# Optimization experiments

Hardware: AMD Instinct MI355X
Metric: run time of the kernel (lower is better)

## Reference

```python
import jax, jax.numpy as jnp
import numpy as np

B, C, H, W = 2, 256, 64, 64
HEADS, SR = 8, 4
D = C // HEADS          # head dim = 32
N = H * W               # query length = 4096
EPS = 1e-5


def _conv(x, w, stride=1, pad=0, groups=1, b=None):
    out = jax.lax.conv_general_dilated(
        x, w, (stride, stride), [(pad, pad), (pad, pad)],
        dimension_numbers=('NCHW', 'OIHW', 'NCHW'),
        feature_group_count=groups)
    if b is not None:
        out = out + b[None, :, None, None]
    return out


def _bn(x, p):
    # p: [4, C] = (gamma, beta, running_mean, running_var), eval-mode BN
    g, b, m, v = p[0], p[1], p[2], p[3]
    s = g / jnp.sqrt(v + EPS)
    return (x - m[None, :, None, None]) * s[None, :, None, None] + b[None, :, None, None]


def setup_inputs() -> dict:
    key = jax.random.key(0)
    ks = iter(jax.random.split(key, 32))
    nrm = lambda shape, s=0.05: jax.random.normal(next(ks), shape, jnp.float32) * s
    def bnp():
        return jnp.stack([jnp.ones((C,), jnp.float32), jnp.zeros((C,), jnp.float32),
                          jax.random.normal(next(ks), (C,), jnp.float32) * 0.1,
                          jax.random.uniform(next(ks), (C,), jnp.float32) + 0.5])
    return dict(
        x=jax.random.normal(next(ks), (B, C, H, W), jnp.float32),
        relative_pos_enc=jax.random.normal(next(ks), (B, 2, 64, 64), jnp.float32),
        q_w=nrm((C, C, 1, 1)), q_b=jnp.zeros((C,), jnp.float32),
        kv_w=nrm((2 * C, C, 1, 1)), kv_b=jnp.zeros((2 * C,), jnp.float32),
        sr1_dw_w=nrm((C, 1, SR + 3, SR + 3)), sr1_bn1=bnp(),
        sr1_pw_w=nrm((C, 1, 1, 1), 0.5), sr1_bn2=bnp(),
        sr2_dw_w=nrm((C, 1, SR // 2 + 3, SR // 2 + 3)), sr2_bn1=bnp(),
        sr2_pw_w=nrm((C, 1, 1, 1), 0.5), sr2_bn2=bnp(),
        local_w=nrm((C, 1, 3, 3)), local_b=jnp.zeros((C,), jnp.float32),
    )


def reference(x, relative_pos_enc, q_w, q_b, kv_w, kv_b,
              sr1_dw_w, sr1_bn1, sr1_pw_w, sr1_bn2,
              sr2_dw_w, sr2_bn1, sr2_pw_w, sr2_bn2,
              local_w, local_b):
    scale = D ** -0.5
    # q: 1x1 conv -> [B, heads, N, D]; both branches use the FIRST half of heads
    q = _conv(x, q_w, b=q_b).reshape(B, HEADS, D, N).transpose(0, 1, 3, 2)
    qh = q[:, :HEADS // 2]

    def branch(dw_w, bn1, pw_w, bn2, stride, pad, rpe_slice):
        # SR path: depthwise conv + BN + ReLU, depthwise 1x1 + BN
        y = jax.nn.relu(_bn(_conv(x, dw_w, stride, pad, groups=C), bn1))
        y = _bn(_conv(y, pw_w, groups=C), bn2)
        # local 3x3 depthwise mixing with residual
        y = _conv(y, local_w, pad=1, groups=C, b=local_b) + y
        kv = _conv(y, kv_w, b=kv_b)                # [B, 2C, h', w']
        k, v = jnp.split(kv, 2, axis=1)
        L = 2 * y.shape[2] * y.shape[3]            # channel-fold doubles kv length
        k = k.reshape(B, HEADS // 2, D, L)
        v = v.reshape(B, HEADS // 2, D, L).transpose(0, 1, 3, 2)
        attn = jnp.einsum('bhnd,bhdl->bhnl', qh, k) * scale
        rpe = jax.image.resize(rpe_slice, (B, 1, N, L), method='bicubic')
        attn = jax.nn.softmax(attn + rpe, axis=-1)
        return jnp.einsum('bhnl,bhld->bhnd', attn, v)

    x1 = branch(sr1_dw_w, sr1_bn1, sr1_pw_w, sr1_bn2,
                SR, (SR + 3) // 2, relative_pos_enc[:, 0:1])
    x2 = branch(sr2_dw_w, sr2_bn1, sr2_pw_w, sr2_bn2,
                SR // 2, (SR // 2 + 3) // 2, relative_pos_enc[:, 1:2])
    out = jnp.concatenate([x1, x2], axis=-1)       # [B, heads//2, N, 2D]
    return out.reshape(B, C, H, W)
```

## Files before the change

### kernel.cpp

```cpp
#include <hip/hip_runtime.h>
#include <hip/hip_bf16.h>
#include <math.h>

#define NB 2
#define NC 256
#define HWIN 4096
#define NN 4096
#define ND 32
#define NHH 4
#define EPSV 1e-5f

typedef short short8 __attribute__((ext_vector_type(8)));
typedef float f32x4 __attribute__((ext_vector_type(4)));
typedef unsigned short u16;
typedef unsigned int u32;

#define OFF_T1   0
#define OFF_T2   262144
#define OFF_Q    1310720
#define OFF_KT1  1835008
#define OFF_VT1  1900544
#define OFF_KT2  1966080
#define OFF_VT2  2228224
#define OFF_RCT1 2490368
#define OFF_RCT2 2531328
#define OFF_WT   2695168
#define OFF_QWT  5054464
#define OFF_LWP  5087232

#define QSCALE 0.2550437314857726f
#define LOG2E  1.4426950408889634f

__device__ __forceinline__ u16 f2bf(float x) {
  unsigned u = __float_as_uint(x);
  u += 0x7fffu + ((u >> 16) & 1u);
  return (u16)(u >> 16);
}

__device__ __forceinline__ u32 pk_bf16(float a, float b) {
  __hip_bfloat162 h = __float22bfloat162_rn(make_float2(a, b));
  u32 r; __builtin_memcpy(&r, &h, 4);
  return r;
}

__device__ __forceinline__ float keysw(float t) {
  t = fabsf(t);
  float w;
  if (t < 1.f)       w = ((1.5f*t - 2.5f)*t)*t + 1.f;
  else if (t < 2.f)  w = ((-0.5f*t + 2.5f)*t - 4.f)*t + 2.f;
  else               w = 0.f;
  return w;
}

template<int KS, int STR, int PAD, int OH>
__device__ __forceinline__ void dwconv_body(int idx, const float* __restrict__ x,
    const float* __restrict__ dww, const float* __restrict__ bn1,
    const float* __restrict__ pww, const float* __restrict__ bn2,
    float* __restrict__ tout) {
  const int hw = OH*OH;
  int s = idx % hw; int c = (idx/hw) % NC; int b = idx/(hw*NC);
  int oy = s / OH, ox = s % OH;
  const float* xp = x + (b*NC + c)*HWIN;
  const float* wp = dww + c*KS*KS;
  float acc = 0.f;
  #pragma unroll
  for (int ky = 0; ky < KS; ++ky) {
    int iy = oy*STR - PAD + ky;
    if (iy < 0 || iy >= 64) continue;
    #pragma unroll
    for (int kx = 0; kx < KS; ++kx) {
      int ix = ox*STR - PAD + kx;
      if (ix < 0 || ix >= 64) continue;
      acc += xp[iy*64 + ix] * wp[ky*KS + kx];
    }
  }
  float s1 = bn1[c] * rsqrtf(bn1[3*NC + c] + EPSV);
  float z = (acc - bn1[2*NC + c])*s1 + bn1[NC + c];
  z = fmaxf(z, 0.f);
  float s2 = bn2[c] * rsqrtf(bn2[3*NC + c] + EPSV);
  z = z * (pww[c]*s2) + (bn2[NC + c] - bn2[2*NC + c]*s2);
  tout[((size_t)(b*hw + s))*NC + c] = z;
}

__device__ __forceinline__ void rpe_body(int idx, const float* __restrict__ rpe,
                                         u16* __restrict__ rcT, int L, int ch) {
  int r = idx & 63; int l = (idx >> 6) % L; int b = idx / (64*L);
  float f = ((float)l + 0.5f)*(64.f/(float)L) - 0.5f;
  int i0 = (int)floorf(f) - 1;
  const float* rp = rpe + ((b*2 + ch)*64 + r)*64;
  float v = 0.f, wsum = 0.f;
  #pragma unroll
  for (int j = 0; j < 4; ++j) {
    int i = i0 + j;
    if (i >= 0 && i < 64) {
      float w = keysw(f - (float)i);
      v += w * rp[i]; wsum += w;
    }
  }
  rcT[((size_t)(b*L + l))*80 + 4 + r] = f2bf(v / wsum);
}

__global__ void __launch_bounds__(256) prep_kernel(
    const float* __restrict__ x,
    const float* __restrict__ dw1, const float* __restrict__ bn11,
    const float* __restrict__ pw1, const float* __restrict__ bn12, float* __restrict__ t1,
    const float* __restrict__ dw2, const float* __restrict__ bn21,
    const float* __restrict__ pw2, const float* __restrict__ bn22, float* __restrict__ t2,
    const float* __restrict__ kvw, float* __restrict__ wtp,
    const float* __restrict__ qw, float* __restrict__ qwp2,
    const float* __restrict__ lw, float* __restrict__ lwp) {
  int blk = blockIdx.x;
  int t = threadIdx.x;
  if (blk < 512) {
    dwconv_body<7,4,3,16>(blk*256 + t, x, dw1, bn11, pw1, bn12, t1);
  } else if (blk < 2560) {
    dwconv_body<5,2,2,32>((blk-512)*256 + t, x, dw2, bn21, pw2, bn22, t2);
  } else if (blk < 2688) {
    int idx = (blk-2560)*256 + t;
    float4 vv = *(const float4*)(kvw + (size_t)idx*4);
    int o = idx >> 6, c4 = idx & 63;
    *(float4*)(wtp + ((size_t)(c4*512 + o))*4) = vv;
  } else if (blk < 2720) {
    int idx = (blk-2688)*256 + t;
    float4 vv = *(const float4*)(qw + (size_t)idx*4);
    int oc = idx >> 6, c0 = (idx & 63)*4;
    int ocq = oc >> 2, r = oc & 3;
    qwp2[((size_t)((c0+0)*32 + ocq))*4 + r] = vv.x;
    qwp2[((size_t)((c0+1)*32 + ocq))*4 + r] = vv.y;
    qwp2[((size_t)((c0+2)*32 + ocq))*4 + r] = vv.z;
    qwp2[((size_t)((c0+3)*32 + ocq))*4 + r] = vv.w;
  } else {
    int c = t;
    #pragma unroll
    for (int tp = 0; tp < 9; ++tp) lwp[tp*256 + c] = lw[c*9 + tp];
  }
}

__global__ void __launch_bounds__(256) localkv_kernel(
    const float* __restrict__ t1T, const float* __restrict__ t2T,
    const float* __restrict__ lwp, const float* __restrict__ lb,
    const float* __restrict__ wtp, const float* __restrict__ kvb,
    u16* __restrict__ kt1, u16* __restrict__ vt1,
    u16* __restrict__ kt2, u16* __restrict__ vt2,
    const float* __restrict__ x, const float* __restrict__ qwp2,
    const float* __restrict__ qb, u16* __restrict__ q,
    const float* __restrict__ rpe, u16* __restrict__ rct1, u16* __restrict__ rct2) {
  __shared__ float sbuf[128*32];
  int blk = blockIdx.x, tid = threadIdx.x;
  if (blk < 640) {
    int kv = blk & 1, ti = blk >> 1;
    const float* tT; u16 *kT, *vT; int OH, hw, b, s0;
    if (ti < 64) { tT = t1T; kT = kt1; vT = vt1; OH = 16; hw = 256;  b = ti >> 5; s0 = (ti & 31)*8; }
    else { int v2 = ti-64; tT = t2T; kT = kt2; vT = vt2; OH = 32; hw = 1024; b = v2 >> 7; s0 = (v2 & 127)*8; }
    int oy = s0 / OH, ox0 = s0 % OH;
    const float* tb = tT + (size_t)b*hw*NC;
    int cl = tid & 63, spg = tid >> 6;
    int c0 = cl*4;
    f32x4 wt9[9];
    #pragma unroll
    for (int tp = 0; tp < 9; ++tp) wt9[tp] = *(const f32x4*)(lwp + tp*256 + c0);
    f32x4 lb4 = *(const f32x4*)(lb + c0);
    #pragma unroll
    for (int i = 0; i < 2; ++i) {
      int sp = spg*2 + i;
      int ox = ox0 + sp;
      f32x4 a = lb4;
      #pragma unroll
      for (int dy = 0; dy < 3; ++dy) {
        int iy = oy + dy - 1;
        if (iy < 0 || iy >= OH) continue;
        #pragma unroll
        for (int dx = 0; dx < 3; ++dx) {
          int ix = ox + dx - 1;
          if (ix < 0 || ix >= OH) continue;
          f32x4 tv = *(const f32x4*)(tb + (size_t)(iy*OH + ix)*NC + c0);
          a += tv * wt9[dy*3 + dx];
        }
      }
      a += *(const f32x4*)(tb + (size_t)(oy*OH + ox)*NC + c0);
      *(f32x4*)(sbuf + sp*NC + c0) = a;
    }
    __syncthreads();
    int ol = tid & 127, sph = tid >> 7;
    int o0i = kv*256 + ol, o1i = o0i + 128;
    float acc0[4], acc1[4];
    float b0 = kvb[o0i], b1 = kvb[o1i];
    #pragma unroll
    for (int i = 0; i < 4; ++i) { acc0[i] = b0; acc1[i] = b1; }
    #pragma unroll 2
    for (int c4 = 0; c4 < 64; ++c4) {
      f32x4 w0 = *(const f32x4*)(wtp + ((size_t)(c4*512 + o0i))*4);
      f32x4 w1 = *(const f32x4*)(wtp + ((size_t)(c4*512 + o1i))*4);
      #pragma unroll
      for (int i = 0; i < 4; ++i) {
        f32x4 y4 = *(const f32x4*)(sbuf + (sph*4 + i)*NC + c4*4);
        #pragma unroll
        for (int j = 0; j < 4; ++j) { acc0[i] += w0[j]*y4[j]; acc1[i] += w1[j]*y4[j]; }
      }
    }
    int L2 = 2*hw;
    #pragma unroll
    for (int k = 0; k < 2; ++k) {
      const float* ap = k ? acc1 : acc0;
      int oo = ol + k*128;
      int hh = oo >> 6, r = oo & 63, d = r >> 1, e = r & 1;
      if (kv == 0) {
        u16* kp = kT + ((size_t)((b*NHH + hh)*L2 + e*hw + s0 + sph*4))*ND + d;
        #pragma unroll
        for (int j = 0; j < 4; ++j) kp[j*ND] = f2bf(ap[j]);
      } else {
        int l0v = e*hw + s0 + sph*4;
        u16* vp = vT + ((size_t)((b*NHH + hh)*(L2/64) + (l0v >> 6))*ND + d)*64 + (l0v & 63);
        #pragma unroll
        for (int j = 0; j < 4; ++j) vp[j] = f2bf(ap[j]);
      }
    }
  } else if (blk < 896) {
    int qblk = blk - 640;
    int b = qblk >> 7;
    int n0 = (qblk & 127) * 32;
    const float* xb = x + (size_t)b*NC*HWIN + n0;
    int ocq = tid & 31, spg = tid >> 5;
    float acc[4][4];
    #pragma unroll
    for (int k = 0; k < 4; ++k) {
      float bias = qb[ocq*4 + k];
      #pragma unroll
      for (int i = 0; i < 4; ++i) acc[k][i] = bias;
    }
    #pragma unroll
    for (int half = 0; half < 2; ++half) {
      #pragma unroll
      for (int j = 0; j < 4; ++j) {
        int u = tid + 256*j;
        int c = u >> 3, spq = u & 7;
        *(f32x4*)(sbuf + c*32 + spq*4) =
            *(const f32x4*)(xb + (size_t)(half*128 + c)*HWIN + spq*4);
      }
      __syncthreads();
      #pragma unroll 4
      for (int c = 0; c < 128; ++c) {
        int cg = half*128 + c;
        f32x4 w4 = *(const f32x4*)(qwp2 + ((size_t)(cg*32 + ocq))*4);
        f32x4 y4 = *(const f32x4*)(sbuf + c*32 + spg*4);
        #pragma unroll
        for (int k = 0; k < 4; ++k)
          #pragma unroll
          for (int i = 0; i < 4; ++i) acc[k][i] += w4[k]*y4[i];
      }
      __syncthreads();
    }
    #pragma unroll
    for (int k = 0; k < 4; ++k) {
      int oc = ocq*4 + k;
      int h = oc >> 5, d = oc & 31;
      u16* qp = q + (((size_t)(b*NHH + h))*NN + n0 + spg*4)*ND + d;
      #pragma unroll
      for (int i = 0; i < 4; ++i) qp[i*ND] = f2bf(acc[k][i]*QSCALE);
    }
  } else if (blk < 1152) {
    rpe_body((blk-896)*256 + tid, rpe, rct1, 512, 0);
  } else {
    rpe_body((blk-1152)*256 + tid, rpe, rct2, 2048, 1);
  }
}

__global__ void __launch_bounds__(256) attn_kernel(
    const u16* __restrict__ qbf,
    const u16* __restrict__ kt1, const u16* __restrict__ vt1, const u16* __restrict__ rct1,
    const u16* __restrict__ kt2, const u16* __restrict__ vt2, const u16* __restrict__ rct2,
    float* __restrict__ out) {
  __shared__ u16 kbuf[64*32];
  __shared__ u16 vbuf[32*64];
  __shared__ u32 pbuf_all[4][16*32];
  int u = blockIdx.x;
  int b = u >> 8, hh = (u >> 6) & 3, rb = u & 63;
  int tid = threadIdx.x;
  int w = tid >> 6, lane = tid & 63;
  int g = lane >> 4, lo = lane & 15;
  u32* pbuf = pbuf_all[w];
  u16* pbuf16 = (u16*)pbuf;
  int n = rb*64 + w*16 + lo;

  short8 qf = *(const short8*)(qbf + (((size_t)(b*NHH + hh))*NN + n)*ND + 8*g);

  float fr = ((float)n + 0.5f)*(1.f/64.f) - 0.5f;
  int ri0 = (int)floorf(fr) - 1;
  int a = (w < 2) ? rb - 2 : rb - 1;
  int rmin = a & ~3;
  float wr4[4]; float wsum = 0.f;
  #pragma unroll
  for (int j = 0; j < 4; ++j) {
    int i = ri0 + j;
    float wv = (i >= 0 && i < 64) ? keysw(fr - (float)i) : 0.f;
    wr4[j] = wv; wsum += wv;
  }
  float invw = LOG2E / wsum;
  float wt8[8];
  #pragma unroll
  for (int s = 0; s < 8; ++s) {
    float acc = 0.f;
    #pragma unroll
    for (int j = 0; j < 4; ++j)
      acc += (ri0 + j - rmin == s) ? wr4[j]*invw : 0.f;
    wt8[s] = acc;
  }
  short8 wtf;
  {
    u32 p0 = pk_bf16(wt8[0], wt8[1]), p1 = pk_bf16(wt8[2], wt8[3]);
    u32 p2 = pk_bf16(wt8[4], wt8[5]), p3 = pk_bf16(wt8[6], wt8[7]);
    uint4 uu = make_uint4(p0, p1, p2, p3);
    wtf = __builtin_bit_cast(short8, uu);
    if (g != 0) wtf = (short8)0;
  }

  const f32x4 zero = {0.f, 0.f, 0.f, 0.f};

  int kr_row = tid >> 2, kr_col = (tid & 3)*8;
  int kr_sw  = ((kr_row >> 1) & 3)*8;
  int vr_row = tid >> 3, vr_col = (tid & 7)*8;
  int vr_sw  = (vr_row & 7)*8;
  int ksw = ((lo >> 1) & 3)*8;
  int vsw = (lo & 7)*8;
  int psw4 = (lo & 7)*4;
  int psw8 = (lo & 7)*8;

  for (int pass = 0; pass < 2; ++pass) {
    const int L  = pass ? 2048 : 512;
    const int nt = pass ? 32 : 8;
    const u16* kbase  = (pass ? kt2 : kt1) + (size_t)(b*NHH + hh)*L*ND;
    const u16* vbase  = (pass ? vt2 : vt1) + (size_t)(b*NHH + hh)*ND*L;
    const u16* rcrow0 = (pass ? rct2 : rct1) + (size_t)b*L*80 + (rmin + 4);

    auto stageLoad = [&](short8& kr, short8& vr, int l0) {
      kr = *(const short8*)(kbase + (size_t)(l0 + kr_row)*ND + kr_col);
      vr = *(const short8*)(vbase + (size_t)(l0 >> 6)*(ND*64) + vr_row*64 + vr_col);
    };
    auto stageStore = [&](short8 kr, short8 vr) {
      *(short8*)(kbuf + kr_row*32 + (kr_col ^ kr_sw)) = kr;
      *(short8*)(vbuf + vr_row*64 + (vr_col ^ vr_sw)) = vr;
    };
    auto loadRC = [&](uint4 (&rc)[4], int l0) {
      #pragma unroll
      for (int c = 0; c < 4; ++c) {
        const u16* arow = rcrow0 + (size_t)(l0 + 16*c + lo)*80;
        uint2 ra = *(const uint2*)arow;
        uint2 rb2 = *(const uint2*)(arow + 4);
        rc[c] = make_uint4(ra.x, ra.y, rb2.x, rb2.y);
      }
    };

    float ssum = 0.f;
    f32x4 o0 = zero, o1 = zero;
    short8 kr, vr;
    uint4 rcA[4], rcB[4];
    stageLoad(kr, vr, 0);
    loadRC(rcA, 0);

    for (int t = 0; t < nt; ++t) {
      stageStore(kr, vr);
      __syncthreads();
      if (t < nt-1) { stageLoad(kr, vr, (t+1)*64); loadRC(rcB, (t+1)*64); }
      f32x4 s4[4];
      #pragma unroll
      for (int c = 0; c < 4; ++c) {
        short8 rcf = __builtin_bit_cast(short8, rcA[c]);
        f32x4 accr = __builtin_amdgcn_mfma_f32_16x16x32_bf16(rcf, wtf, zero, 0, 0, 0);
        short8 kf = *(const short8*)(kbuf + (16*c + lo)*32 + ((8*g) ^ ksw));
        s4[c] = __builtin_amdgcn_mfma_f32_16x16x32_bf16(kf, qf, accr, 0, 0, 0);
      }
      float psum = 0.f;
      u32 pk[8];
      #pragma unroll
      for (int c = 0; c < 4; ++c) {
        float p0 = __builtin_amdgcn_exp2f(s4[c][0]);
        float p1 = __builtin_amdgcn_exp2f(s4[c][1]);
        float p2 = __builtin_amdgcn_exp2f(s4[c][2]);
        float p3 = __builtin_amdgcn_exp2f(s4[c][3]);
        psum += (p0 + p1) + (p2 + p3);
        pk[2*c]   = pk_bf16(p0, p1);
        pk[2*c+1] = pk_bf16(p2, p3);
      }
      ssum += psum;
      #pragma unroll
      for (int c = 0; c < 4; ++c)
        *(uint2*)(pbuf + lo*32 + ((8*c + 2*g) ^ psw4)) = make_uint2(pk[2*c], pk[2*c+1]);
      short8 pf0 = *(const short8*)(pbuf16 + lo*64 + ((8*g) ^ psw8));
      short8 pf1 = *(const short8*)(pbuf16 + lo*64 + ((32 + 8*g) ^ psw8));
      short8 v00 = *(const short8*)(vbuf + lo*64 + ((8*g) ^ vsw));
      short8 v01 = *(const short8*)(vbuf + lo*64 + ((32 + 8*g) ^ vsw));
      short8 v10 = *(const short8*)(vbuf + (16 + lo)*64 + ((8*g) ^ vsw));
      short8 v11 = *(const short8*)(vbuf + (16 + lo)*64 + ((32 + 8*g) ^ vsw));
      o0 = __builtin_amdgcn_mfma_f32_16x16x32_bf16(v00, pf0, o0, 0, 0, 0);
      o1 = __builtin_amdgcn_mfma_f32_16x16x32_bf16(v10, pf0, o1, 0, 0, 0);
      o0 = __builtin_amdgcn_mfma_f32_16x16x32_bf16(v01, pf1, o0, 0, 0, 0);
      o1 = __builtin_amdgcn_mfma_f32_16x16x32_bf16(v11, pf1, o1, 0, 0, 0);
      if (t < nt-1) {
        #pragma unroll
        for (int j = 0; j < 4; ++j) rcA[j] = rcB[j];
      }
      __syncthreads();
    }

    ssum += __shfl_xor(ssum, 16, 64);
    ssum += __shfl_xor(ssum, 32, 64);
    float inv = 1.f/ssum;
    f32x4 w0 = o0*inv, w1 = o1*inv;
    float* op = out + ((size_t)((b*NC + hh*64 + rb)*64 + (w*16 + lo)))*64 + pass*32;
    *(f32x4*)(op + 4*g)      = w0;
    *(f32x4*)(op + 16 + 4*g) = w1;
  }
}

extern "C" void kernel_launch(void* const* d_in, const int* in_sizes, int n_in,
                              void* d_out, int out_size, void* d_ws, size_t ws_size,
                              hipStream_t stream) {
  const float* x    = (const float*)d_in[0];
  const float* rpe  = (const float*)d_in[1];
  const float* qw   = (const float*)d_in[2];
  const float* qb   = (const float*)d_in[3];
  const float* kvw  = (const float*)d_in[4];
  const float* kvb  = (const float*)d_in[5];
  const float* dw1  = (const float*)d_in[6];
  const float* bn11 = (const float*)d_in[7];
  const float* pw1  = (const float*)d_in[8];
  const float* bn12 = (const float*)d_in[9];
  const float* dw2  = (const float*)d_in[10];
  const float* bn21 = (const float*)d_in[11];
  const float* pw2  = (const float*)d_in[12];
  const float* bn22 = (const float*)d_in[13];
  const float* lw   = (const float*)d_in[14];
  const float* lb   = (const float*)d_in[15];
  float* out = (float*)d_out;
  float* ws  = (float*)d_ws;

  float* t1   = ws + OFF_T1;
  float* t2   = ws + OFF_T2;
  u16*   q    = (u16*)(ws + OFF_Q);
  u16*   kt1  = (u16*)(ws + OFF_KT1);
  u16*   vt1  = (u16*)(ws + OFF_VT1);
  u16*   kt2  = (u16*)(ws + OFF_KT2);
  u16*   vt2  = (u16*)(ws + OFF_VT2);
  u16*   rct1 = (u16*)(ws + OFF_RCT1);
  u16*   rct2 = (u16*)(ws + OFF_RCT2);
  float* wtp  = ws + OFF_WT;
  float* qwp2 = ws + OFF_QWT;
  float* lwp  = ws + OFF_LWP;

  hipLaunchKernelGGL(prep_kernel, dim3(2721), dim3(256), 0, stream,
                     x, dw1, bn11, pw1, bn12, t1, dw2, bn21, pw2, bn22, t2,
                     kvw, wtp, qw, qwp2, lw, lwp);
  hipLaunchKernelGGL(localkv_kernel, dim3(2176), dim3(256), 0, stream,
                     t1, t2, lwp, lb, wtp, kvb, kt1, vt1, kt2, vt2, x, qwp2, qb, q,
                     rpe, rct1, rct2);
  hipLaunchKernelGGL(attn_kernel, dim3(512), dim3(256), 0, stream,
                     q, kt1, vt1, rct1, kt2, vt2, rct2, out);
}
```

Baseline: 180.5 us.

## Split attention kernel into per-branch 2-wave blocks for more parallelism

Each attention block used to process 64 queries with 4 waves and loop over both branches in sequence. Now each block handles 32 queries and a single branch with 2 waves, and the long branch's blocks are scheduled first. The grid grows from 512 to 2048 blocks, which should fill the GPU better and balance the uneven branch lengths. In exchange, each K/V tile is staged into shared memory by fewer queries, so K/V global traffic per query rises. Each thread now loads two K and two V vectors per tile.

```diff
diff --git a/kernel.cpp b/kernel.cpp
--- a/kernel.cpp
+++ b/kernel.cpp
@@ -265,28 +265,38 @@
   }
 }
 
-__global__ void __launch_bounds__(256) attn_kernel(
+__global__ void __launch_bounds__(128) attn_kernel(
     const u16* __restrict__ qbf,
     const u16* __restrict__ kt1, const u16* __restrict__ vt1, const u16* __restrict__ rct1,
     const u16* __restrict__ kt2, const u16* __restrict__ vt2, const u16* __restrict__ rct2,
     float* __restrict__ out) {
   __shared__ u16 kbuf[64*32];
   __shared__ u16 vbuf[32*64];
-  __shared__ u32 pbuf_all[4][16*32];
+  __shared__ u32 pbuf_all[2][16*32];
   int u = blockIdx.x;
-  int b = u >> 8, hh = (u >> 6) & 3, rb = u & 63;
+  int br, b, hh, rb;
+  if (u < 1024) { br = 1; b = u >> 9; hh = (u >> 7) & 3; rb = u & 127; }
+  else { int v = u - 1024; br = 0; b = v >> 9; hh = (v >> 7) & 3; rb = v & 127; }
+  const int L  = br ? 2048 : 512;
+  const int nt = br ? 32 : 8;
+  const u16* kT  = br ? kt2 : kt1;
+  const u16* vT  = br ? vt2 : vt1;
+  const u16* rcT = br ? rct2 : rct1;
   int tid = threadIdx.x;
   int w = tid >> 6, lane = tid & 63;
   int g = lane >> 4, lo = lane & 15;
   u32* pbuf = pbuf_all[w];
   u16* pbuf16 = (u16*)pbuf;
-  int n = rb*64 + w*16 + lo;
+  int n = rb*32 + w*16 + lo;
+
+  const u16* kbase = kT + (size_t)(b*NHH + hh)*L*ND;
+  const u16* vbase = vT + (size_t)(b*NHH + hh)*ND*L;
 
   short8 qf = *(const short8*)(qbf + (((size_t)(b*NHH + hh))*NN + n)*ND + 8*g);
 
   float fr = ((float)n + 0.5f)*(1.f/64.f) - 0.5f;
   int ri0 = (int)floorf(fr) - 1;
-  int a = (w < 2) ? rb - 2 : rb - 1;
+  int a = ((rb - 1) >> 1) - 1;
   int rmin = a & ~3;
   float wr4[4]; float wsum = 0.f;
   #pragma unroll
@@ -313,8 +323,11 @@
     wtf = __builtin_bit_cast(short8, uu);
     if (g != 0) wtf = (short8)0;
   }
+  const u16* rcrow0 = rcT + (size_t)b*L*80 + (rmin + 4);
 
   const f32x4 zero = {0.f, 0.f, 0.f, 0.f};
+  float ssum = 0.f;
+  f32x4 o0 = zero, o1 = zero;
 
   int kr_row = tid >> 2, kr_col = (tid & 3)*8;
   int kr_sw  = ((kr_row >> 1) & 3)*8;
@@ -325,91 +338,87 @@
   int psw4 = (lo & 7)*4;
   int psw8 = (lo & 7)*8;
 
-  for (int pass = 0; pass < 2; ++pass) {
-    const int L  = pass ? 2048 : 512;
-    const int nt = pass ? 32 : 8;
-    const u16* kbase  = (pass ? kt2 : kt1) + (size_t)(b*NHH + hh)*L*ND;
-    const u16* vbase  = (pass ? vt2 : vt1) + (size_t)(b*NHH + hh)*ND*L;
-    const u16* rcrow0 = (pass ? rct2 : rct1) + (size_t)b*L*80 + (rmin + 4);
-
-    auto stageLoad = [&](short8& kr, short8& vr, int l0) {
-      kr = *(const short8*)(kbase + (size_t)(l0 + kr_row)*ND + kr_col);
-      vr = *(const short8*)(vbase + (size_t)(l0 >> 6)*(ND*64) + vr_row*64 + vr_col);
-    };
-    auto stageStore = [&](short8 kr, short8 vr) {
-      *(short8*)(kbuf + kr_row*32 + (kr_col ^ kr_sw)) = kr;
-      *(short8*)(vbuf + vr_row*64 + (vr_col ^ vr_sw)) = vr;
-    };
-    auto loadRC = [&](uint4 (&rc)[4], int l0) {
-      #pragma unroll
-      for (int c = 0; c < 4; ++c) {
-        const u16* arow = rcrow0 + (size_t)(l0 + 16*c + lo)*80;
-        uint2 ra = *(const uint2*)arow;
-        uint2 rb2 = *(const uint2*)(arow + 4);
-        rc[c] = make_uint4(ra.x, ra.y, rb2.x, rb2.y);
-      }
-    };
-
-    float ssum = 0.f;
-    f32x4 o0 = zero, o1 = zero;
-    short8 kr, vr;
-    uint4 rcA[4], rcB[4];
-    stageLoad(kr, vr, 0);
-    loadRC(rcA, 0);
-
-    for (int t = 0; t < nt; ++t) {
-      stageStore(kr, vr);
-      __syncthreads();
-      if (t < nt-1) { stageLoad(kr, vr, (t+1)*64); loadRC(rcB, (t+1)*64); }
-      f32x4 s4[4];
-      #pragma unroll
-      for (int c = 0; c < 4; ++c) {
-        short8 rcf = __builtin_bit_cast(short8, rcA[c]);
-        f32x4 accr = __builtin_amdgcn_mfma_f32_16x16x32_bf16(rcf, wtf, zero, 0, 0, 0);
-        short8 kf = *(const short8*)(kbuf + (16*c + lo)*32 + ((8*g) ^ ksw));
-        s4[c] = __builtin_amdgcn_mfma_f32_16x16x32_bf16(kf, qf, accr, 0, 0, 0);
-      }
-      float psum = 0.f;
-      u32 pk[8];
-      #pragma unroll
-      for (int c = 0; c < 4; ++c) {
-        float p0 = __builtin_amdgcn_exp2f(s4[c][0]);
-        float p1 = __builtin_amdgcn_exp2f(s4[c][1]);
-        float p2 = __builtin_amdgcn_exp2f(s4[c][2]);
-        float p3 = __builtin_amdgcn_exp2f(s4[c][3]);
-        psum += (p0 + p1) + (p2 + p3);
-        pk[2*c]   = pk_bf16(p0, p1);
-        pk[2*c+1] = pk_bf16(p2, p3);
-      }
-      ssum += psum;
-      #pragma unroll
-      for (int c = 0; c < 4; ++c)
-        *(uint2*)(pbuf + lo*32 + ((8*c + 2*g) ^ psw4)) = make_uint2(pk[2*c], pk[2*c+1]);
-      short8 pf0 = *(const short8*)(pbuf16 + lo*64 + ((8*g) ^ psw8));
-      short8 pf1 = *(const short8*)(pbuf16 + lo*64 + ((32 + 8*g) ^ psw8));
-      short8 v00 = *(const short8*)(vbuf + lo*64 + ((8*g) ^ vsw));
-      short8 v01 = *(const short8*)(vbuf + lo*64 + ((32 + 8*g) ^ vsw));
-      short8 v10 = *(const short8*)(vbuf + (16 + lo)*64 + ((8*g) ^ vsw));
-      short8 v11 = *(const short8*)(vbuf + (16 + lo)*64 + ((32 + 8*g) ^ vsw));
-      o0 = __builtin_amdgcn_mfma_f32_16x16x32_bf16(v00, pf0, o0, 0, 0, 0);
-      o1 = __builtin_amdgcn_mfma_f32_16x16x32_bf16(v10, pf0, o1, 0, 0, 0);
-      o0 = __builtin_amdgcn_mfma_f32_16x16x32_bf16(v01, pf1, o0, 0, 0, 0);
-      o1 = __builtin_amdgcn_mfma_f32_16x16x32_bf16(v11, pf1, o1, 0, 0, 0);
-      if (t < nt-1) {
-        #pragma unroll
-        for (int j = 0; j < 4; ++j) rcA[j] = rcB[j];
-      }
-      __syncthreads();
-    }
-
-    ssum += __shfl_xor(ssum, 16, 64);
-    ssum += __shfl_xor(ssum, 32, 64);
-    float inv = 1.f/ssum;
-    f32x4 w0 = o0*inv, w1 = o1*inv;
-    float* op = out + ((size_t)((b*NC + hh*64 + rb)*64 + (w*16 + lo)))*64 + pass*32;
-    *(f32x4*)(op + 4*g)      = w0;
-    *(f32x4*)(op + 16 + 4*g) = w1;
-  }
+  auto stageLoad = [&](short8& k0, short8& k1, short8& v0, short8& v1, int l0) {
+    k0 = *(const short8*)(kbase + (size_t)(l0 + kr_row)*ND + kr_col);
+    k1 = *(const short8*)(kbase + (size_t)(l0 + kr_row + 32)*ND + kr_col);
+    const u16* vt = vbase + (size_t)(l0 >> 6)*(ND*64);
+    v0 = *(const short8*)(vt + vr_row*64 + vr_col);
+    v1 = *(const short8*)(vt + (vr_row + 16)*64 + vr_col);
+  };
+  auto stageStore = [&](short8 k0, short8 k1, short8 v0, short8 v1) {
+    *(short8*)(kbuf + kr_row*32 + (kr_col ^ kr_sw)) = k0;
+    *(short8*)(kbuf + (kr_row + 32)*32 + (kr_col ^ kr_sw)) = k1;
+    *(short8*)(vbuf + vr_row*64 + (vr_col ^ vr_sw)) = v0;
+    *(short8*)(vbuf + (vr_row + 16)*64 + (vr_col ^ vr_sw)) = v1;
+  };
+  auto loadRC = [&](uint4 (&rc)[4], int l0) {
+    #pragma unroll
+    for (int c = 0; c < 4; ++c) {
+      const u16* arow = rcrow0 + (size_t)(l0 + 16*c + lo)*80;
+      uint2 ra = *(const uint2*)arow;
+      uint2 rb2 = *(const uint2*)(arow + 4);
+      rc[c] = make_uint4(ra.x, ra.y, rb2.x, rb2.y);
+    }
+  };
+
+  short8 k0r, k1r, v0r, v1r;
+  uint4 rcA[4], rcB[4];
+  stageLoad(k0r, k1r, v0r, v1r, 0);
+  loadRC(rcA, 0);
+
+  for (int t = 0; t < nt; ++t) {
+    stageStore(k0r, k1r, v0r, v1r);
+    __syncthreads();
+    if (t < nt-1) { stageLoad(k0r, k1r, v0r, v1r, (t+1)*64); loadRC(rcB, (t+1)*64); }
+    f32x4 s4[4];
+    #pragma unroll
+    for (int c = 0; c < 4; ++c) {
+      short8 rcf = __builtin_bit_cast(short8, rcA[c]);
+      f32x4 accr = __builtin_amdgcn_mfma_f32_16x16x32_bf16(rcf, wtf, zero, 0, 0, 0);
+      short8 kf = *(const short8*)(kbuf + (16*c + lo)*32 + ((8*g) ^ ksw));
+      s4[c] = __builtin_amdgcn_mfma_f32_16x16x32_bf16(kf, qf, accr, 0, 0, 0);
+    }
+    float psum = 0.f;
+    u32 pk[8];
+    #pragma unroll
+    for (int c = 0; c < 4; ++c) {
+      float p0 = __builtin_amdgcn_exp2f(s4[c][0]);
+      float p1 = __builtin_amdgcn_exp2f(s4[c][1]);
+      float p2 = __builtin_amdgcn_exp2f(s4[c][2]);
+      float p3 = __builtin_amdgcn_exp2f(s4[c][3]);
+      psum += (p0 + p1) + (p2 + p3);
+      pk[2*c]   = pk_bf16(p0, p1);
+      pk[2*c+1] = pk_bf16(p2, p3);
+    }
+    ssum += psum;
+    #pragma unroll
+    for (int c = 0; c < 4; ++c)
+      *(uint2*)(pbuf + lo*32 + ((8*c + 2*g) ^ psw4)) = make_uint2(pk[2*c], pk[2*c+1]);
+    short8 pf0 = *(const short8*)(pbuf16 + lo*64 + ((8*g) ^ psw8));
+    short8 pf1 = *(const short8*)(pbuf16 + lo*64 + ((32 + 8*g) ^ psw8));
+    short8 v00 = *(const short8*)(vbuf + lo*64 + ((8*g) ^ vsw));
+    short8 v01 = *(const short8*)(vbuf + lo*64 + ((32 + 8*g) ^ vsw));
+    short8 v10 = *(const short8*)(vbuf + (16 + lo)*64 + ((8*g) ^ vsw));
+    short8 v11 = *(const short8*)(vbuf + (16 + lo)*64 + ((32 + 8*g) ^ vsw));
+    o0 = __builtin_amdgcn_mfma_f32_16x16x32_bf16(v00, pf0, o0, 0, 0, 0);
+    o1 = __builtin_amdgcn_mfma_f32_16x16x32_bf16(v10, pf0, o1, 0, 0, 0);
+    o0 = __builtin_amdgcn_mfma_f32_16x16x32_bf16(v01, pf1, o0, 0, 0, 0);
+    o1 = __builtin_amdgcn_mfma_f32_16x16x32_bf16(v11, pf1, o1, 0, 0, 0);
+    if (t < nt-1) {
+      #pragma unroll
+      for (int j = 0; j < 4; ++j) rcA[j] = rcB[j];
+    }
+    __syncthreads();
+  }
+
+  ssum += __shfl_xor(ssum, 16, 64);
+  ssum += __shfl_xor(ssum, 32, 64);
+  float inv = 1.f/ssum;
+  f32x4 w0 = o0*inv, w1 = o1*inv;
+  float* op = out + ((size_t)((b*NC + hh*64 + (rb >> 1))*64 +
+                              ((rb & 1)*32 + w*16 + lo)))*64 + (br ? 32 : 0);
+  *(f32x4*)(op + 4*g)      = w0;
+  *(f32x4*)(op + 16 + 4*g) = w1;
 }
 
 extern "C" void kernel_launch(void* const* d_in, const int* in_sizes, int n_in,
@@ -453,6 +462,6 @@
   hipLaunchKernelGGL(localkv_kernel, dim3(2176), dim3(256), 0, stream,
                      t1, t2, lwp, lb, wtp, kvb, kt1, vt1, kt2, vt2, x, qwp2, qb, q,
                      rpe, rct1, rct2);
-  hipLaunchKernelGGL(attn_kernel, dim3(512), dim3(256), 0, stream,
+  hipLaunchKernelGGL(attn_kernel, dim3(2048), dim3(128), 0, stream,
                      q, kt1, vt1, rct1, kt2, vt2, rct2, out);
 }
```

Result: no change. 178.6 us (-1.1%).
